# Kernel tuning notes

Hardware: AMD Instinct MI355X
Metric: run time of the kernel (lower is better)

The kernel has to match this reference:

```python
import jax, jax.numpy as jnp
import numpy as np

NSPECIES = 7
NRBF = 16
RCR, RCA, RMIN = 0.51, 0.35, 0.08
ETA_R = 1970.0   # nm^-2 (~19.7 A^-2)
ETA_A = 800.0    # nm^-2 (~8 A^-2)
ZETA = 32.0
N_SHFA, N_SHFZ = 8, 4
SUBLEN = N_SHFA * N_SHFZ
NPAIRS_SP = NSPECIES * (NSPECIES + 1) // 2  # 28
SHFR = jnp.asarray(np.linspace(RMIN, RCR, NRBF, endpoint=False), jnp.float32)
SHFA = jnp.asarray(np.linspace(RMIN, RCA, N_SHFA, endpoint=False), jnp.float32)
SHFZ = jnp.asarray(np.linspace(0.0, np.pi, N_SHFZ, endpoint=False) + np.pi / (2 * N_SHFZ), jnp.float32)

def _triu_index(ns):
    s1, s2 = np.triu_indices(ns)
    t = np.zeros((ns, ns), np.int32)
    pi = np.arange(len(s1), dtype=np.int32)
    t[s1, s2] = pi
    t[s2, s1] = pi
    return jnp.asarray(t)

TRIU = _triu_index(NSPECIES)

def _cutoff(d, rc):
    return jnp.where(d <= rc, 0.5 * (jnp.cos(d * (np.pi / rc)) + 1.0), 0.0)

def setup_inputs() -> dict:
    rng = np.random.default_rng(0)
    n_mol, M, L = 4000, 24, 0.9
    pos = rng.uniform(0.0, L, (n_mol, M, 3)).astype(np.float32)
    iu, ju = np.triu_indices(M, 1)
    rvec = pos[:, ju] - pos[:, iu]              # [n_mol, Pm, 3], r_ij = pos_j - pos_i
    dist = np.linalg.norm(rvec, axis=-1)
    keep = (dist > 0.02) & (dist < RCR)
    mol, pidx = np.nonzero(keep)
    pair_indices = np.stack([mol * M + iu[pidx], mol * M + ju[pidx]]).astype(np.int32)
    r_ij = rvec[mol, pidx].astype(np.float32)
    d_ij = dist[mol, pidx].astype(np.float32)[:, None]
    species = rng.integers(0, NSPECIES, n_mol * M).astype(np.int32)
    # pairs within angular cutoff (mirrors even_closer_indices)
    close_idx = np.nonzero(d_ij[:, 0] <= RCA)[0].astype(np.int32)
    # triple_by_molecule on the filtered pair list
    ai12 = pair_indices[:, close_idx]
    n = ai12.shape[1]
    ai1 = ai12.reshape(-1)
    order = np.argsort(ai1, kind='stable').astype(np.int64)
    sorted_ai1 = ai1[order]
    uniq, counts = np.unique(sorted_ai1, return_counts=True)
    pair_sizes = counts * (counts - 1) // 2
    central_atom_index = np.repeat(uniq, pair_sizes).astype(np.int32)
    starts = np.concatenate([[0], np.cumsum(counts)[:-1]])
    cmax = int(counts.max())
    ti, tj = np.triu_indices(cmax, 1)
    valid = tj[None, :] < counts[:, None]
    gi = (starts[:, None] + ti[None, :])[valid]
    gj = (starts[:, None] + tj[None, :])[valid]
    local12 = order[np.stack([gi, gj])]         # [2, T]
    sign12 = np.where(local12 < n, 1, -1).astype(np.int32)
    pair_index12 = (local12 % n).astype(np.int32)
    return {
        'd_ij': jnp.asarray(d_ij), 'r_ij': jnp.asarray(r_ij),
        'pair_indices': jnp.asarray(pair_indices), 'species': jnp.asarray(species),
        'close_idx': jnp.asarray(close_idx),
        'central_atom_index': jnp.asarray(central_atom_index),
        'pair_index12': jnp.asarray(pair_index12), 'sign12': jnp.asarray(sign12),
        'num_atoms': n_mol * M,
    }

def reference(d_ij, r_ij, pair_indices, species, close_idx, central_atom_index, pair_index12, sign12, num_atoms):
    d = d_ij[:, 0]                                                # [P]
    # radial symmetry functions * cosine cutoff
    rfv = 0.25 * jnp.exp(-ETA_R * (d[:, None] - SHFR) ** 2) * _cutoff(d, RCR)[:, None]  # [P,16]
    sp12 = species[pair_indices]                                  # [2,P]
    idx12 = pair_indices * NSPECIES + sp12[::-1]                  # [2,P]
    radial_aev = jnp.zeros((num_atoms * NSPECIES, NRBF), rfv.dtype)
    radial_aev = radial_aev.at[idx12[0]].add(rfv).at[idx12[1]].add(rfv)
    radial_aev = radial_aev.reshape(num_atoms, NSPECIES * NRBF)
    # angular preprocessing (gather filtered pairs into triples)
    ai12c = pair_indices[:, close_idx]
    sp12c = species[ai12c]                                        # [2,Pc]
    rijc = r_ij[close_idx]                                        # [Pc,3]
    sp12s = sp12c[:, pair_index12]                                # [2,2,T]
    rij12 = rijc[pair_index12] * sign12[..., None].astype(rijc.dtype)  # [2,T,3]
    sp12_ = jnp.where(sign12 == 1, sp12s[1], sp12s[0])            # [2,T]
    # angular symmetry functions (TorchANI-style)
    v1, v2 = rij12[0], rij12[1]
    d1 = jnp.linalg.norm(v1, axis=-1)
    d2 = jnp.linalg.norm(v2, axis=-1)
    cosang = 0.95 * jnp.sum(v1 * v2, -1) / (d1 * d2)
    ang = jnp.arccos(cosang)
    fcj = _cutoff(d1, RCA) * _cutoff(d2, RCA)
    f1 = ((1.0 + jnp.cos(ang[:, None] - SHFZ)) * 0.5) ** ZETA     # [T,4]
    f2 = jnp.exp(-ETA_A * ((d1 + d2)[:, None] * 0.5 - SHFA) ** 2) # [T,8]
    ang_terms = 2.0 * (f2[:, :, None] * f1[:, None, :]).reshape(-1, SUBLEN) * fcj[:, None]
    # scatter into per-atom, per-species-pair slots
    idx = central_atom_index * NPAIRS_SP + TRIU[sp12_[0], sp12_[1]]
    ang_aev = jnp.zeros((num_atoms * NPAIRS_SP, SUBLEN), ang_terms.dtype).at[idx].add(ang_terms)
    ang_aev = ang_aev.reshape(num_atoms, NPAIRS_SP * SUBLEN)
    return jnp.concatenate([radial_aev, ang_aev], axis=-1)        # [N, 112+896]
```

## Files before the change

### kernel.cpp

```cpp
#include <hip/hip_runtime.h>
#include <math.h>

#define NSPECIES 7
#define NRBF 16
#define SUBLEN 32
#define ROWLEN 1008
#define ANG_OFF 112
#define RADLEN 112
#define ANGLEN 896
#define M_ATOMS 24
#define APC 8
#define MAXPAIR 276

typedef float v4f __attribute__((ext_vector_type(4)));

__global__ void setup_kernel(const float* __restrict__ r_ij,
                             const int* __restrict__ pair_indices,
                             const int* __restrict__ species,
                             const int* __restrict__ close_idx,
                             const int* __restrict__ central_atom_index,
                             const int* __restrict__ pair_index12,
                             const int* __restrict__ sign12,
                             v4f* __restrict__ t_rec, int* __restrict__ t_dst,
                             int* __restrict__ pstart, int* __restrict__ tstart,
                             int P, int T, int nmol, int ngrp) {
    int t = blockIdx.x * blockDim.x + threadIdx.x;

    if (t <= P) {
        int m  = (t < P) ? pair_indices[t] / M_ATOMS : nmol;
        int mp = (t > 0) ? pair_indices[t - 1] / M_ATOMS : -1;
        for (int v = mp + 1; v <= m; ++v) pstart[v] = t;
    }
    if (t <= T) {
        int g  = (t < T) ? (central_atom_index[t] >> 3) : ngrp;
        int gp = (t > 0) ? (central_atom_index[t - 1] >> 3) : -1;
        for (int v = gp + 1; v <= g; ++v) tstart[v] = t;
    }
    if (t < T) {
        int p1 = pair_index12[t];
        int p2 = pair_index12[T + t];
        int s1 = sign12[t];
        int s2 = sign12[T + t];
        int ca = central_atom_index[t];
        int gp1 = close_idx[p1];
        int gp2 = close_idx[p2];

        float sg1 = (float)s1, sg2 = (float)s2;
        float v1x = r_ij[gp1 * 3 + 0] * sg1;
        float v1y = r_ij[gp1 * 3 + 1] * sg1;
        float v1z = r_ij[gp1 * 3 + 2] * sg1;
        float v2x = r_ij[gp2 * 3 + 0] * sg2;
        float v2y = r_ij[gp2 * 3 + 1] * sg2;
        float v2z = r_ij[gp2 * 3 + 2] * sg2;

        int spa = species[pair_indices[(s1 == 1 ? P : 0) + gp1]];
        int spb = species[pair_indices[(s2 == 1 ? P : 0) + gp2]];

        float d1 = sqrtf(v1x * v1x + v1y * v1y + v1z * v1z);
        float d2 = sqrtf(v2x * v2x + v2y * v2y + v2z * v2z);
        float dot = v1x * v2x + v1y * v2y + v1z * v2z;

        float cosang = 0.95f * dot / (d1 * d2);
        float sinang = sqrtf(fmaxf(1.0f - cosang * cosang, 0.0f));

        float fc1 = (d1 <= 0.35f) ? 0.5f * (__cosf(d1 * (float)(M_PI / 0.35)) + 1.0f) : 0.0f;
        float fc2 = (d2 <= 0.35f) ? 0.5f * (__cosf(d2 * (float)(M_PI / 0.35)) + 1.0f) : 0.0f;

        int lo = min(spa, spb), hi = max(spa, spb);
        int triu = lo * NSPECIES - (lo * (lo - 1)) / 2 + (hi - lo);

        v4f rec;
        rec.x = (d1 + d2) * 0.5f;
        rec.y = 2.0f * fc1 * fc2;
        rec.z = cosang;
        rec.w = sinang;
        t_rec[t] = rec;
        t_dst[t] = (ca << 5) | triu;
    }
}

__global__ __launch_bounds__(256) void radial_kernel(
        const float* __restrict__ d_ij,
        const int* __restrict__ pair_indices,
        const int* __restrict__ species,
        const int* __restrict__ pstart,
        float* __restrict__ out, int P, int natoms) {
    __shared__ float rows[M_ATOMS * RADLEN];
    __shared__ v4f stage[MAXPAIR];

    int tid = threadIdx.x;
    int mol = blockIdx.x;
    int base = mol * M_ATOMS;
    if (base >= natoms) return;

    int p_lo = pstart[mol];
    int p_hi = pstart[mol + 1];
    int np = p_hi - p_lo;

    v4f z = {0.f, 0.f, 0.f, 0.f};
    v4f* r4 = (v4f*)rows;
    for (int c = tid; c < M_ATOMS * RADLEN / 4; c += 256) r4[c] = z;

    for (int k = tid; k < np; k += 256) {
        int p = p_lo + k;
        float d = d_ij[p];
        int i = pair_indices[p];
        int j = pair_indices[P + p];
        int si = species[i];
        int sj = species[j];
        float fc = (d <= 0.51f) ? 0.5f * (__cosf(d * (float)(M_PI / 0.51)) + 1.0f) : 0.0f;
        v4f s;
        s.x = d;
        s.y = 0.25f * fc;
        s.z = __int_as_float(((i - base) << 3) | sj);
        s.w = __int_as_float(((j - base) << 3) | si);
        stage[k] = s;
    }
    __syncthreads();

    int n16 = np * NRBF;
    for (int idx = tid; idx < n16; idx += 256) {
        int pp = idx >> 4;
        int k = idx & 15;
        v4f s = stage[pp];
        float shfr = 0.08f + (float)k * 0.026875f;
        float diff = s.x - shfr;
        float rfv = s.y * __expf(-1970.0f * diff * diff);
        int di = __float_as_int(s.z);
        int dj = __float_as_int(s.w);
        atomicAdd(&rows[(di >> 3) * RADLEN + (di & 7) * NRBF + k], rfv);
        atomicAdd(&rows[(dj >> 3) * RADLEN + (dj & 7) * NRBF + k], rfv);
    }
    __syncthreads();

    v4f* ov = (v4f*)out;
    for (int c = tid; c < M_ATOMS * (RADLEN / 4); c += 256) {
        int r = c / (RADLEN / 4);
        int e = c % (RADLEN / 4);
        if (base + r < natoms) {
            v4f v = r4[c];
            __builtin_nontemporal_store(v, &ov[(size_t)(base + r) * (ROWLEN / 4) + e]);
        }
    }
}

__global__ __launch_bounds__(256) void angular_kernel(
        const v4f* __restrict__ t_rec, const int* __restrict__ t_dst,
        const int* __restrict__ tstart,
        float* __restrict__ out, int natoms) {
    __shared__ float rows[APC * ANGLEN];

    int tid = threadIdx.x;
    int grp = blockIdx.x;
    int base = grp * APC;
    if (base >= natoms) return;

    int t_lo = tstart[grp];
    int t_hi = tstart[grp + 1];

    v4f z = {0.f, 0.f, 0.f, 0.f};
    v4f* r4 = (v4f*)rows;
    for (int c = tid; c < APC * ANGLEN / 4; c += 256) r4[c] = z;
    __syncthreads();

    int n32 = (t_hi - t_lo) * SUBLEN;
    for (int idx = tid; idx < n32; idx += 256) {
        int t = t_lo + (idx >> 5);
        int l = idx & 31;

        v4f rec = t_rec[t];
        int dst = t_dst[t];

        int aa = l >> 2;
        int zz = l & 3;

        float shfa = 0.08f + (float)aa * 0.03375f;
        float dm = rec.x - shfa;
        float f2 = __expf(-800.0f * dm * dm);

        const float c8 = 0.92387953251f;
        const float s8 = 0.38268343236f;
        bool midz = (zz == 1) | (zz == 2);
        float cmag = midz ? s8 : c8;
        float smag = midz ? c8 : s8;
        float cz = (zz >= 2) ? -cmag : cmag;

        float bse = 0.5f * (1.0f + rec.z * cz + rec.w * smag);
        float x = bse * bse;
        x = x * x;
        x = x * x;
        x = x * x;
        x = x * x;

        float term = rec.y * f2 * x;

        int row = (dst >> 5) - base;
        atomicAdd(&rows[row * ANGLEN + (dst & 31) * SUBLEN + l], term);
    }
    __syncthreads();

    v4f* ov = (v4f*)out;
    for (int c = tid; c < APC * (ANGLEN / 4); c += 256) {
        int r = c / (ANGLEN / 4);
        int e = c % (ANGLEN / 4);
        if (base + r < natoms) {
            v4f v = r4[c];
            __builtin_nontemporal_store(v, &ov[(size_t)(base + r) * (ROWLEN / 4) + (ANG_OFF / 4) + e]);
        }
    }
}

extern "C" void kernel_launch(void* const* d_in, const int* in_sizes, int n_in,
                              void* d_out, int out_size, void* d_ws, size_t ws_size,
                              hipStream_t stream) {
    const float* d_ij               = (const float*)d_in[0];
    const float* r_ij               = (const float*)d_in[1];
    const int*   pair_indices       = (const int*)d_in[2];
    const int*   species            = (const int*)d_in[3];
    const int*   close_idx          = (const int*)d_in[4];
    const int*   central_atom_index = (const int*)d_in[5];
    const int*   pair_index12       = (const int*)d_in[6];
    const int*   sign12             = (const int*)d_in[7];
    float* out = (float*)d_out;

    int P      = in_sizes[0];
    int T      = in_sizes[5];
    int natoms = in_sizes[3];
    int nmol   = natoms / M_ATOMS;
    int ngrp   = (natoms + APC - 1) / APC;

    char* w = (char*)d_ws;
    v4f* t_rec  = (v4f*)w;                 w += (size_t)T * 16;
    int* t_dst  = (int*)w;                 w += (size_t)T * 4;
    int* pstart = (int*)w;                 w += (size_t)(nmol + 1) * 4;
    int* tstart = (int*)w;

    int n = max(P, T) + 1;
    setup_kernel<<<(n + 255) / 256, 256, 0, stream>>>(r_ij, pair_indices, species, close_idx,
                                                      central_atom_index, pair_index12, sign12,
                                                      t_rec, t_dst, pstart, tstart,
                                                      P, T, nmol, ngrp);
    radial_kernel<<<nmol, 256, 0, stream>>>(d_ij, pair_indices, species, pstart, out, P, natoms);
    angular_kernel<<<ngrp, 256, 0, stream>>>(t_rec, t_dst, tstart, out, natoms);
}
```

Measured before the change: 215.0 us.

## Fuse radial and angular AEV kernels into one half-molecule block kernel

Merges the radial and angular kernels into a single kernel where each 512-thread block owns 12 atoms (half a molecule) and builds full 1008-float rows in shared memory. Per-triple geometry records are now computed in chunks inside the block instead of being written to and reread from workspace by the setup kernel, which is reduced to building index tables. This removes a kernel launch and the global round-trip of triple records, and each output row is written with one contiguous store. In exchange, each block recomputes radial terms for the whole molecule's pairs and discards the half it does not own. Shared memory use also rises to about 53 KB per block, which may limit occupancy.

```diff
diff --git a/kernel.cpp b/kernel.cpp
--- a/kernel.cpp
+++ b/kernel.cpp
@@ -6,102 +6,62 @@
 #define SUBLEN 32
 #define ROWLEN 1008
 #define ANG_OFF 112
-#define RADLEN 112
-#define ANGLEN 896
 #define M_ATOMS 24
-#define APC 8
-#define MAXPAIR 276
+#define APB 12
+#define THREADS 512
+#define CH 224
+#define MAXPAIR 280
 
 typedef float v4f __attribute__((ext_vector_type(4)));
 
-__global__ void setup_kernel(const float* __restrict__ r_ij,
-                             const int* __restrict__ pair_indices,
-                             const int* __restrict__ species,
-                             const int* __restrict__ close_idx,
-                             const int* __restrict__ central_atom_index,
-                             const int* __restrict__ pair_index12,
-                             const int* __restrict__ sign12,
-                             v4f* __restrict__ t_rec, int* __restrict__ t_dst,
+__global__ void table_kernel(const int* __restrict__ pair_indices,
+                             const int* __restrict__ cai,
                              int* __restrict__ pstart, int* __restrict__ tstart,
-                             int P, int T, int nmol, int ngrp) {
+                             int P, int T, int nmol, int nblk) {
     int t = blockIdx.x * blockDim.x + threadIdx.x;
-
     if (t <= P) {
         int m  = (t < P) ? pair_indices[t] / M_ATOMS : nmol;
         int mp = (t > 0) ? pair_indices[t - 1] / M_ATOMS : -1;
         for (int v = mp + 1; v <= m; ++v) pstart[v] = t;
     }
     if (t <= T) {
-        int g  = (t < T) ? (central_atom_index[t] >> 3) : ngrp;
-        int gp = (t > 0) ? (central_atom_index[t - 1] >> 3) : -1;
+        int g  = (t < T) ? cai[t] / APB : nblk;
+        int gp = (t > 0) ? cai[t - 1] / APB : -1;
         for (int v = gp + 1; v <= g; ++v) tstart[v] = t;
     }
-    if (t < T) {
-        int p1 = pair_index12[t];
-        int p2 = pair_index12[T + t];
-        int s1 = sign12[t];
-        int s2 = sign12[T + t];
-        int ca = central_atom_index[t];
-        int gp1 = close_idx[p1];
-        int gp2 = close_idx[p2];
-
-        float sg1 = (float)s1, sg2 = (float)s2;
-        float v1x = r_ij[gp1 * 3 + 0] * sg1;
-        float v1y = r_ij[gp1 * 3 + 1] * sg1;
-        float v1z = r_ij[gp1 * 3 + 2] * sg1;
-        float v2x = r_ij[gp2 * 3 + 0] * sg2;
-        float v2y = r_ij[gp2 * 3 + 1] * sg2;
-        float v2z = r_ij[gp2 * 3 + 2] * sg2;
-
-        int spa = species[pair_indices[(s1 == 1 ? P : 0) + gp1]];
-        int spb = species[pair_indices[(s2 == 1 ? P : 0) + gp2]];
-
-        float d1 = sqrtf(v1x * v1x + v1y * v1y + v1z * v1z);
-        float d2 = sqrtf(v2x * v2x + v2y * v2y + v2z * v2z);
-        float dot = v1x * v2x + v1y * v2y + v1z * v2z;
-
-        float cosang = 0.95f * dot / (d1 * d2);
-        float sinang = sqrtf(fmaxf(1.0f - cosang * cosang, 0.0f));
-
-        float fc1 = (d1 <= 0.35f) ? 0.5f * (__cosf(d1 * (float)(M_PI / 0.35)) + 1.0f) : 0.0f;
-        float fc2 = (d2 <= 0.35f) ? 0.5f * (__cosf(d2 * (float)(M_PI / 0.35)) + 1.0f) : 0.0f;
-
-        int lo = min(spa, spb), hi = max(spa, spb);
-        int triu = lo * NSPECIES - (lo * (lo - 1)) / 2 + (hi - lo);
-
-        v4f rec;
-        rec.x = (d1 + d2) * 0.5f;
-        rec.y = 2.0f * fc1 * fc2;
-        rec.z = cosang;
-        rec.w = sinang;
-        t_rec[t] = rec;
-        t_dst[t] = (ca << 5) | triu;
-    }
 }
 
-__global__ __launch_bounds__(256) void radial_kernel(
+__global__ __launch_bounds__(THREADS) void aev_fused(
         const float* __restrict__ d_ij,
+        const float* __restrict__ r_ij,
         const int* __restrict__ pair_indices,
         const int* __restrict__ species,
+        const int* __restrict__ close_idx,
+        const int* __restrict__ cai,
+        const int* __restrict__ pair_index12,
+        const int* __restrict__ sign12,
         const int* __restrict__ pstart,
-        float* __restrict__ out, int P, int natoms) {
-    __shared__ float rows[M_ATOMS * RADLEN];
-    __shared__ v4f stage[MAXPAIR];
+        const int* __restrict__ tstart,
+        float* __restrict__ out, int P, int T, int natoms) {
+    __shared__ float rows[APB * ROWLEN];
+    __shared__ __align__(16) float ustage[MAXPAIR * 4];
 
     int tid = threadIdx.x;
-    int mol = blockIdx.x;
-    int base = mol * M_ATOMS;
+    int blk = blockIdx.x;
+    int base = blk * APB;
     if (base >= natoms) return;
-
-    int p_lo = pstart[mol];
-    int p_hi = pstart[mol + 1];
-    int np = p_hi - p_lo;
+    int mol = base / M_ATOMS;
 
     v4f z = {0.f, 0.f, 0.f, 0.f};
     v4f* r4 = (v4f*)rows;
-    for (int c = tid; c < M_ATOMS * RADLEN / 4; c += 256) r4[c] = z;
-
-    for (int k = tid; k < np; k += 256) {
+    for (int c = tid; c < APB * ROWLEN / 4; c += THREADS) r4[c] = z;
+
+    int p_lo = pstart[mol], p_hi = pstart[mol + 1];
+    int t_lo = tstart[blk], t_hi = tstart[blk + 1];
+    int np = p_hi - p_lo;
+
+    v4f* pst = (v4f*)ustage;
+    for (int k = tid; k < np; k += THREADS) {
         int p = p_lo + k;
         float d = d_ij[p];
         int i = pair_indices[p];
@@ -114,99 +74,112 @@
         s.y = 0.25f * fc;
         s.z = __int_as_float(((i - base) << 3) | sj);
         s.w = __int_as_float(((j - base) << 3) | si);
-        stage[k] = s;
+        pst[k] = s;
     }
     __syncthreads();
 
-    int n16 = np * NRBF;
-    for (int idx = tid; idx < n16; idx += 256) {
+    for (int idx = tid; idx < np * NRBF; idx += THREADS) {
         int pp = idx >> 4;
         int k = idx & 15;
-        v4f s = stage[pp];
+        v4f s = pst[pp];
         float shfr = 0.08f + (float)k * 0.026875f;
         float diff = s.x - shfr;
         float rfv = s.y * __expf(-1970.0f * diff * diff);
         int di = __float_as_int(s.z);
         int dj = __float_as_int(s.w);
-        atomicAdd(&rows[(di >> 3) * RADLEN + (di & 7) * NRBF + k], rfv);
-        atomicAdd(&rows[(dj >> 3) * RADLEN + (dj & 7) * NRBF + k], rfv);
+        int li = di >> 3, lj = dj >> 3;
+        if ((unsigned)li < APB) atomicAdd(&rows[li * ROWLEN + (di & 7) * NRBF + k], rfv);
+        if ((unsigned)lj < APB) atomicAdd(&rows[lj * ROWLEN + (dj & 7) * NRBF + k], rfv);
     }
     __syncthreads();
 
-    v4f* ov = (v4f*)out;
-    for (int c = tid; c < M_ATOMS * (RADLEN / 4); c += 256) {
-        int r = c / (RADLEN / 4);
-        int e = c % (RADLEN / 4);
-        if (base + r < natoms) {
-            v4f v = r4[c];
-            __builtin_nontemporal_store(v, &ov[(size_t)(base + r) * (ROWLEN / 4) + e]);
+    v4f* trec = (v4f*)ustage;
+    int* tdst = ((int*)ustage) + CH * 4;
+
+    for (int c0 = t_lo; c0 < t_hi; c0 += CH) {
+        int n = min(CH, t_hi - c0);
+        if (tid < n) {
+            int t = c0 + tid;
+            int p1 = pair_index12[t];
+            int p2 = pair_index12[T + t];
+            int s1 = sign12[t];
+            int s2 = sign12[T + t];
+            int ca = cai[t];
+            int gp1 = close_idx[p1];
+            int gp2 = close_idx[p2];
+
+            float sg1 = (float)s1, sg2 = (float)s2;
+            float v1x = r_ij[gp1 * 3 + 0] * sg1;
+            float v1y = r_ij[gp1 * 3 + 1] * sg1;
+            float v1z = r_ij[gp1 * 3 + 2] * sg1;
+            float v2x = r_ij[gp2 * 3 + 0] * sg2;
+            float v2y = r_ij[gp2 * 3 + 1] * sg2;
+            float v2z = r_ij[gp2 * 3 + 2] * sg2;
+
+            int spa = species[pair_indices[(s1 == 1 ? P : 0) + gp1]];
+            int spb = species[pair_indices[(s2 == 1 ? P : 0) + gp2]];
+
+            float d1 = sqrtf(v1x * v1x + v1y * v1y + v1z * v1z);
+            float d2 = sqrtf(v2x * v2x + v2y * v2y + v2z * v2z);
+            float dot = v1x * v2x + v1y * v2y + v1z * v2z;
+
+            float cosang = 0.95f * dot / (d1 * d2);
+            float sinang = sqrtf(fmaxf(1.0f - cosang * cosang, 0.0f));
+
+            float fc1 = (d1 <= 0.35f) ? 0.5f * (__cosf(d1 * (float)(M_PI / 0.35)) + 1.0f) : 0.0f;
+            float fc2 = (d2 <= 0.35f) ? 0.5f * (__cosf(d2 * (float)(M_PI / 0.35)) + 1.0f) : 0.0f;
+
+            int lo = min(spa, spb), hi = max(spa, spb);
+            int triu = lo * NSPECIES - (lo * (lo - 1)) / 2 + (hi - lo);
+
+            v4f rec;
+            rec.x = (d1 + d2) * 0.5f;
+            rec.y = 2.0f * fc1 * fc2;
+            rec.z = cosang;
+            rec.w = sinang;
+            trec[tid] = rec;
+            tdst[tid] = ((ca - base) << 5) | triu;
         }
-    }
-}
-
-__global__ __launch_bounds__(256) void angular_kernel(
-        const v4f* __restrict__ t_rec, const int* __restrict__ t_dst,
-        const int* __restrict__ tstart,
-        float* __restrict__ out, int natoms) {
-    __shared__ float rows[APC * ANGLEN];
-
-    int tid = threadIdx.x;
-    int grp = blockIdx.x;
-    int base = grp * APC;
-    if (base >= natoms) return;
-
-    int t_lo = tstart[grp];
-    int t_hi = tstart[grp + 1];
-
-    v4f z = {0.f, 0.f, 0.f, 0.f};
-    v4f* r4 = (v4f*)rows;
-    for (int c = tid; c < APC * ANGLEN / 4; c += 256) r4[c] = z;
-    __syncthreads();
-
-    int n32 = (t_hi - t_lo) * SUBLEN;
-    for (int idx = tid; idx < n32; idx += 256) {
-        int t = t_lo + (idx >> 5);
-        int l = idx & 31;
-
-        v4f rec = t_rec[t];
-        int dst = t_dst[t];
-
-        int aa = l >> 2;
-        int zz = l & 3;
-
-        float shfa = 0.08f + (float)aa * 0.03375f;
-        float dm = rec.x - shfa;
-        float f2 = __expf(-800.0f * dm * dm);
-
-        const float c8 = 0.92387953251f;
-        const float s8 = 0.38268343236f;
-        bool midz = (zz == 1) | (zz == 2);
-        float cmag = midz ? s8 : c8;
-        float smag = midz ? c8 : s8;
-        float cz = (zz >= 2) ? -cmag : cmag;
-
-        float bse = 0.5f * (1.0f + rec.z * cz + rec.w * smag);
-        float x = bse * bse;
-        x = x * x;
-        x = x * x;
-        x = x * x;
-        x = x * x;
-
-        float term = rec.y * f2 * x;
-
-        int row = (dst >> 5) - base;
-        atomicAdd(&rows[row * ANGLEN + (dst & 31) * SUBLEN + l], term);
-    }
-    __syncthreads();
-
-    v4f* ov = (v4f*)out;
-    for (int c = tid; c < APC * (ANGLEN / 4); c += 256) {
-        int r = c / (ANGLEN / 4);
-        int e = c % (ANGLEN / 4);
-        if (base + r < natoms) {
-            v4f v = r4[c];
-            __builtin_nontemporal_store(v, &ov[(size_t)(base + r) * (ROWLEN / 4) + (ANG_OFF / 4) + e]);
+        __syncthreads();
+
+        for (int idx = tid; idx < n * SUBLEN; idx += THREADS) {
+            int tt = idx >> 5;
+            int l = idx & 31;
+            v4f rec = trec[tt];
+            int dst = tdst[tt];
+
+            int aa = l >> 2;
+            int zz = l & 3;
+
+            float shfa = 0.08f + (float)aa * 0.03375f;
+            float dm = rec.x - shfa;
+            float f2 = __expf(-800.0f * dm * dm);
+
+            const float c8 = 0.92387953251f;
+            const float s8 = 0.38268343236f;
+            bool midz = (zz == 1) | (zz == 2);
+            float cmag = midz ? s8 : c8;
+            float smag = midz ? c8 : s8;
+            float cz = (zz >= 2) ? -cmag : cmag;
+
+            float bse = 0.5f * (1.0f + rec.z * cz + rec.w * smag);
+            float x = bse * bse;
+            x = x * x;
+            x = x * x;
+            x = x * x;
+            x = x * x;
+
+            float term = rec.y * f2 * x;
+            atomicAdd(&rows[(dst >> 5) * ROWLEN + ANG_OFF + (dst & 31) * SUBLEN + l], term);
         }
+        __syncthreads();
+    }
+
+    int nrows = min(APB, natoms - base);
+    v4f* ov = (v4f*)(out + (size_t)base * ROWLEN);
+    for (int c = tid; c < nrows * (ROWLEN / 4); c += THREADS) {
+        v4f v = r4[c];
+        __builtin_nontemporal_store(v, &ov[c]);
     }
 }
 
@@ -227,19 +200,15 @@
     int T      = in_sizes[5];
     int natoms = in_sizes[3];
     int nmol   = natoms / M_ATOMS;
-    int ngrp   = (natoms + APC - 1) / APC;
-
-    char* w = (char*)d_ws;
-    v4f* t_rec  = (v4f*)w;                 w += (size_t)T * 16;
-    int* t_dst  = (int*)w;                 w += (size_t)T * 4;
-    int* pstart = (int*)w;                 w += (size_t)(nmol + 1) * 4;
-    int* tstart = (int*)w;
+    int nblk   = (natoms + APB - 1) / APB;
+
+    int* pstart = (int*)d_ws;
+    int* tstart = pstart + (nmol + 1);
 
     int n = max(P, T) + 1;
-    setup_kernel<<<(n + 255) / 256, 256, 0, stream>>>(r_ij, pair_indices, species, close_idx,
-                                                      central_atom_index, pair_index12, sign12,
-                                                      t_rec, t_dst, pstart, tstart,
-                                                      P, T, nmol, ngrp);
-    radial_kernel<<<nmol, 256, 0, stream>>>(d_ij, pair_indices, species, pstart, out, P, natoms);
-    angular_kernel<<<ngrp, 256, 0, stream>>>(t_rec, t_dst, tstart, out, natoms);
+    table_kernel<<<(n + 255) / 256, 256, 0, stream>>>(pair_indices, central_atom_index,
+                                                      pstart, tstart, P, T, nmol, nblk);
+    aev_fused<<<nblk, THREADS, 0, stream>>>(d_ij, r_ij, pair_indices, species, close_idx,
+                                            central_atom_index, pair_index12, sign12,
+                                            pstart, tstart, out, P, T, natoms);
 }
```

After: 221.5 us. 1.03x slower.
